# Optimization experiments

Measured on AMD Instinct MI355X. Metric: run time of the kernel, lower is better.

## Reference

```python
import jax, jax.numpy as jnp
import numpy as np


def setup_inputs() -> dict:
    key = jax.random.key(0)
    k0, k1, k2 = jax.random.split(key, 3)
    B, S, E, U = 32, 2048, 512, 512
    return {
        "seq": jax.random.normal(k0, (B, S, E), jnp.float32),
        "w1": jax.random.normal(k1, (U, E), jnp.float32) * 0.05,
        "b1": jnp.zeros((U,), jnp.float32),
        "w2": jax.random.normal(k2, (3, U), jnp.float32) * 0.05,
        "b2": jnp.zeros((3,), jnp.float32),
        "num_lists": 16,
        "list_size": 16,
    }


def reference(seq, w1, b1, w2, b2, num_lists, list_size):
    B, S, E = seq.shape
    # action decoder: Linear -> SiLU -> Linear -> Softmax over 3 actions
    h = jax.nn.silu(jnp.einsum('bse,ue->bsu', seq, w1) + b1)
    actions = jax.nn.softmax(jnp.einsum('bsu,au->bsa', h, w2) + b2, axis=-1)  # (B,S,3)

    Hn, Wn = num_lists, list_size
    T0 = jnp.zeros((B, Hn, Wn), seq.dtype).at[:, 0, -1].set(1.0)   # superposition grid
    rs0 = jnp.zeros((B, Hn), seq.dtype).at[:, 0].set(1.0)          # row sums

    # process actions in reverse token order; scan over seq dim
    acts_rev = jnp.swapaxes(actions[:, ::-1, :], 0, 1)  # (S,B,3)

    def step(carry, a):
        T, rs = carry
        a0, a1, a2 = a[:, 0:1], a[:, 1:2], a[:, 2:3]  # each (B,1)
        # weight used to place the current (reversed) token: (a0+a1)*T
        w_step = (a0 + a1)[:, :, None] * T  # (B,H,W)
        # devolve: the grouped conv2d with kernel [0, a2, a0] is a width-shift blend
        other = a2[:, :, None] * T[:, :, :-1] + a0[:, :, None] * T[:, :, 1:]  # cols 0..W-2
        sums = a1 * jnp.roll(rs, 1, axis=1).at[:, 0].set(0.0)                 # (B,H)
        last = sums + a2 * T[:, :, -1]                                        # (B,H)
        rs_new = (a0 + a2) * rs + sums
        T_new = jnp.concatenate([other, last[:, :, None]], axis=2)
        return (T_new, rs_new), w_step

    _, ws = jax.lax.scan(step, (T0, rs0), acts_rev)  # ws: (S,B,H,W), aligned with reversed seq
    # G = sum_i w_i[...,None] * token_i[:,None,None,:]
    G = jnp.einsum('sbhw,bse->bhwe', ws, seq[:, ::-1, :])
    return G
```

## Files before the change

kernel.cpp:

```cpp
#include <hip/hip_runtime.h>
#include <stdint.h>

#define S_LEN 2048
#define NB 32
#define NE 512
#define NU 512
#define NP 256

typedef __bf16 bf16;
typedef __bf16 bf16x8 __attribute__((ext_vector_type(8)));
typedef __bf16 bf16x4 __attribute__((ext_vector_type(4)));
typedef float f32x4 __attribute__((ext_vector_type(4)));
typedef float f32x8 __attribute__((ext_vector_type(8)));

__device__ __forceinline__ void gload16(const void* g, void* l) {
    __builtin_amdgcn_global_load_lds(
        (__attribute__((address_space(1))) void*)g,
        (__attribute__((address_space(3))) void*)l, 16, 0, 0);
}

__device__ __forceinline__ float dpp_shr1_z(float x) {
    return __builtin_bit_cast(float, __builtin_amdgcn_update_dpp(
        0, __builtin_bit_cast(int, x), 0x111, 0xF, 0xF, true));
}
__device__ __forceinline__ float dpp_shl1_z(float x) {
    return __builtin_bit_cast(float, __builtin_amdgcn_update_dpp(
        0, __builtin_bit_cast(int, x), 0x101, 0xF, 0xF, true));
}

__device__ __forceinline__ void stage_tile(const bf16* __restrict__ src, int SR,
                                           bf16* lds, int tid) {
#pragma unroll
    for (int rnd = 0; rnd < 2; ++rnd) {
        const int c = rnd * 256 + tid;
        const int row = c >> 2;
        const int q = (c & 3) ^ ((c >> 3) & 3);
        gload16(src + (size_t)row * SR + q * 8, lds + c * 8);
    }
}

__global__ __launch_bounds__(256) void k_wconv(
    const float* __restrict__ w1, bf16* __restrict__ wHi, bf16* __restrict__ wLo)
{
    const int i = (blockIdx.x * 256 + threadIdx.x) * 4;
    const float4 v = *(const float4*)(w1 + i);
    const float vv[4] = {v.x, v.y, v.z, v.w};
    bf16x4 oh, ol;
#pragma unroll
    for (int q = 0; q < 4; ++q) {
        const bf16 hb = (bf16)vv[q];
        oh[q] = hb;
        ol[q] = (bf16)(vv[q] - (float)hb);
    }
    *(bf16x4*)(wHi + i) = oh;
    *(bf16x4*)(wLo + i) = ol;
}

__global__ __launch_bounds__(256, 2) void k_gemm1(
    const float* __restrict__ seq,
    const bf16* __restrict__ w1H, const bf16* __restrict__ w1L,
    const float* __restrict__ b1v, const float* __restrict__ w2,
    const float* __restrict__ b2v, float* __restrict__ actions)
{
    __shared__ __align__(16) bf16 BhL[2][4096];
    __shared__ __align__(16) bf16 BlL[2][4096];
    const int tid = threadIdx.x;
    const int wid = tid >> 6;
    const int lane = tid & 63;
    const int lr = lane & 15, lg = lane >> 4;
    const int m0 = blockIdx.x << 7;

    const float* arow0 = seq + (size_t)(m0 + wid * 32 + lr) * NE + lg * 8;
    const float* arow1 = arow0 + 16 * NE;
    const int lroff = lr * 64 + (lg ^ ((lr >> 1) & 3)) * 16;

    float plog[3][2][4];
#pragma unroll
    for (int a = 0; a < 3; ++a)
#pragma unroll
        for (int i = 0; i < 2; ++i)
#pragma unroll
            for (int q = 0; q < 4; ++q) plog[a][i][q] = 0.f;

    f32x4 acc[2][8];
    stage_tile(w1H, NE, BhL[0], tid);
    stage_tile(w1L, NE, BlL[0], tid);
    f32x8 Aa0 = *(const f32x8*)(arow0);
    f32x8 Aa1 = *(const f32x8*)(arow1);
    f32x8 Ab0, Ab1;

#define G1_BODY(g, buf, Ac0, Ac1, An0, An1) do {                              \
        __syncthreads();                                                      \
        if (((g) & 15) == 0) {                                                \
            _Pragma("unroll") for (int i = 0; i < 2; ++i)                     \
            _Pragma("unroll") for (int j = 0; j < 8; ++j)                     \
                acc[i][j] = (f32x4)(0.f);                                     \
        }                                                                     \
        bf16x8 bh[8], bl[8];                                                  \
        _Pragma("unroll") for (int j = 0; j < 8; ++j) {                       \
            bh[j] = *(const bf16x8*)((const char*)BhL[buf] + j * 1024 + lroff);\
            bl[j] = *(const bf16x8*)((const char*)BlL[buf] + j * 1024 + lroff);\
        }                                                                     \
        __syncthreads();                                                      \
        if ((g) < 63) {                                                       \
            const int gn = (g) + 1;                                           \
            const int u0n = (gn >> 4) << 7;                                   \
            const int k0n = (gn & 15) << 5;                                   \
            An0 = *(const f32x8*)(arow0 + k0n);                               \
            An1 = *(const f32x8*)(arow1 + k0n);                               \
            stage_tile(w1H + (size_t)u0n * NE + k0n, NE, BhL[(buf) ^ 1], tid);\
            stage_tile(w1L + (size_t)u0n * NE + k0n, NE, BlL[(buf) ^ 1], tid);\
        }                                                                     \
        bf16x8 Ah0, Al0, Ah1, Al1;                                            \
        _Pragma("unroll") for (int q = 0; q < 8; ++q) {                       \
            const bf16 h0 = (bf16)Ac0[q];                                     \
            Ah0[q] = h0; Al0[q] = (bf16)(Ac0[q] - (float)h0);                 \
            const bf16 h1 = (bf16)Ac1[q];                                     \
            Ah1[q] = h1; Al1[q] = (bf16)(Ac1[q] - (float)h1);                 \
        }                                                                     \
        _Pragma("unroll") for (int j = 0; j < 8; ++j) {                       \
            acc[0][j] = __builtin_amdgcn_mfma_f32_16x16x32_bf16(Ah0, bh[j], acc[0][j], 0, 0, 0); \
            acc[0][j] = __builtin_amdgcn_mfma_f32_16x16x32_bf16(Ah0, bl[j], acc[0][j], 0, 0, 0); \
            acc[0][j] = __builtin_amdgcn_mfma_f32_16x16x32_bf16(Al0, bh[j], acc[0][j], 0, 0, 0); \
            acc[1][j] = __builtin_amdgcn_mfma_f32_16x16x32_bf16(Ah1, bh[j], acc[1][j], 0, 0, 0); \
            acc[1][j] = __builtin_amdgcn_mfma_f32_16x16x32_bf16(Ah1, bl[j], acc[1][j], 0, 0, 0); \
            acc[1][j] = __builtin_amdgcn_mfma_f32_16x16x32_bf16(Al1, bh[j], acc[1][j], 0, 0, 0); \
        }                                                                     \
        if (((g) & 15) == 15) {                                               \
            const int u0 = ((g) >> 4) << 7;                                   \
            _Pragma("unroll") for (int j = 0; j < 8; ++j) {                   \
                const int col = u0 + j * 16 + lr;                             \
                const float b1c = b1v[col];                                   \
                const float w20 = w2[col], w21 = w2[NU + col], w22 = w2[2 * NU + col]; \
                _Pragma("unroll") for (int i = 0; i < 2; ++i)                 \
                _Pragma("unroll") for (int q = 0; q < 4; ++q) {               \
                    const float x = acc[i][j][q] + b1c;                       \
                    const float hgate = x / (1.f + __expf(-x));               \
                    plog[0][i][q] = fmaf(hgate, w20, plog[0][i][q]);          \
                    plog[1][i][q] = fmaf(hgate, w21, plog[1][i][q]);          \
                    plog[2][i][q] = fmaf(hgate, w22, plog[2][i][q]);          \
                }                                                             \
            }                                                                 \
        }                                                                     \
    } while (0)

    for (int gg = 0; gg < 32; ++gg) {
        G1_BODY(2 * gg, 0, Aa0, Aa1, Ab0, Ab1);
        G1_BODY(2 * gg + 1, 1, Ab0, Ab1, Aa0, Aa1);
    }
#undef G1_BODY

#pragma unroll
    for (int m = 1; m < 16; m <<= 1) {
#pragma unroll
        for (int a = 0; a < 3; ++a)
#pragma unroll
            for (int i = 0; i < 2; ++i)
#pragma unroll
                for (int q = 0; q < 4; ++q)
                    plog[a][i][q] += __shfl_xor(plog[a][i][q], m);
    }
    const float bb0 = b2v[0], bb1 = b2v[1], bb2 = b2v[2];
    if (lr == 0) {
#pragma unroll
        for (int i = 0; i < 2; ++i)
#pragma unroll
            for (int q = 0; q < 4; ++q) {
                const int row = m0 + wid * 32 + i * 16 + lg * 4 + q;
                const float l0 = plog[0][i][q] + bb0;
                const float l1 = plog[1][i][q] + bb1;
                const float l2 = plog[2][i][q] + bb2;
                const float mx = fmaxf(l0, fmaxf(l1, l2));
                const float e0 = __expf(l0 - mx), e1 = __expf(l1 - mx), e2 = __expf(l2 - mx);
                const float inv = 1.f / (e0 + e1 + e2);
                *(float4*)(actions + (size_t)row * 4) = make_float4(e0 * inv, e1 * inv, e2 * inv, 0.f);
            }
    }
}

union SPMem {
    float tile[64][65];
    struct {
        float4 actbuf[3][256];
        float  sums[2][256][16];
    } s;
};

__device__ __forceinline__ void rs_chunk(const float4* __restrict__ pb,
                                         float* __restrict__ so,
                                         float& rs, int lane)
{
    for (int w = 0; w < 32; ++w) {
        const int rtop = 255 - w * 8;
        const float4 e0 = pb[rtop],     e1 = pb[rtop - 1];
        const float4 e2 = pb[rtop - 2], e3 = pb[rtop - 3];
        const float4 e4 = pb[rtop - 4], e5 = pb[rtop - 5];
        const float4 e6 = pb[rtop - 6], e7 = pb[rtop - 7];
#define RS_STEP(E, k) do {                                                    \
        const float rsp = dpp_shr1_z(rs);                                     \
        const float s = (E).y * rsp;                                          \
        if (lane < 16) so[(rtop - (k)) * 16 + lane] = s;                      \
        rs = fmaf((E).x + (E).z, rs, s);                                      \
    } while (0)
        RS_STEP(e0, 0); RS_STEP(e1, 1); RS_STEP(e2, 2); RS_STEP(e3, 3);
        RS_STEP(e4, 4); RS_STEP(e5, 5); RS_STEP(e6, 6); RS_STEP(e7, 7);
#undef RS_STEP
    }
}

__device__ __forceinline__ void t_chunk(const float4* __restrict__ lb,
                                        const float* __restrict__ sp,
                                        float& T, bf16* __restrict__ obp,
                                        int tbase0, int w15)
{
    for (int w = 0; w < 32; ++w) {
        const int rtop = 255 - w * 8;
        const int tglob = tbase0 + rtop - 7;
        const float4 av0 = lb[rtop],     av1 = lb[rtop - 1];
        const float4 av2 = lb[rtop - 2], av3 = lb[rtop - 3];
        const float4 av4 = lb[rtop - 4], av5 = lb[rtop - 5];
        const float4 av6 = lb[rtop - 6], av7 = lb[rtop - 7];
        const float su0 = sp[rtop * 16],       su1 = sp[(rtop - 1) * 16];
        const float su2 = sp[(rtop - 2) * 16], su3 = sp[(rtop - 3) * 16];
        const float su4 = sp[(rtop - 4) * 16], su5 = sp[(rtop - 5) * 16];
        const float su6 = sp[(rtop - 6) * 16], su7 = sp[(rtop - 7) * 16];
        bf16x8 fr;
#define T_STEP(Av, Su, fi) do {                                               \
        const float a0 = (Av).x, a1 = (Av).y, a2 = (Av).z;                    \
        fr[fi] = (bf16)((a0 + a1) * T);                                       \
        const float nT = dpp_shl1_z(T);                                       \
        const float contrib = w15 ? (Su) : a0 * nT;                           \
        T = fmaf(a2, T, contrib);                                             \
    } while (0)
        T_STEP(av0, su0, 7); T_STEP(av1, su1, 6);
        T_STEP(av2, su2, 5); T_STEP(av3, su3, 4);
        T_STEP(av4, su4, 3); T_STEP(av5, su5, 2);
        T_STEP(av6, su6, 1); T_STEP(av7, su7, 0);
#undef T_STEP
        *(bf16x8*)(obp + tglob) = fr;
    }
}

__global__ __launch_bounds__(320) void k_scan_prep(
    const float* __restrict__ actions, bf16* __restrict__ wsT,
    const float* __restrict__ seq, bf16* __restrict__ tHi)
{
    __shared__ SPMem sm;
    const int tid = threadIdx.x;
    if (blockIdx.x < 32) {
        const int b = blockIdx.x;
        const int wid = tid >> 6;
        const int lane = tid & 63;
        const float4* actb = (const float4*)actions + (size_t)b * S_LEN;

        float rs = (lane == 0) ? 1.f : 0.f;
        float T = (wid == 0 && lane == 15) ? 1.f : 0.f;
        const int w15 = ((lane & 15) == 15) ? 1 : 0;
        bf16* obp = wsT + ((size_t)b * NP + wid * 64 + lane) * S_LEN;

        if (wid < 4) {
            gload16(actb + 1792 + wid * 64 + lane, &sm.s.actbuf[0][wid * 64]);
            gload16(actb + 1536 + wid * 64 + lane, &sm.s.actbuf[1][wid * 64]);
            asm volatile("s_waitcnt vmcnt(0)" ::: "memory");
        }
        __syncthreads();
        if (wid == 4) rs_chunk(sm.s.actbuf[0], &sm.s.sums[0][0][0], rs, lane);
        __syncthreads();

        int bufT = 0, bufP = 1, bufL = 2;
        for (int c = 0; c < 8; ++c) {
            if (wid < 4) {
                if (c < 6)
                    gload16(actb + (1280 - c * 256) + wid * 64 + lane,
                            &sm.s.actbuf[bufL][wid * 64]);
                t_chunk(sm.s.actbuf[bufT],
                        &sm.s.sums[c & 1][0][wid * 4 + (lane >> 4)],
                        T, obp, 1792 - c * 256, w15);
                asm volatile("s_waitcnt vmcnt(0)" ::: "memory");
            } else {
                if (c < 7)
                    rs_chunk(sm.s.actbuf[bufP], &sm.s.sums[(c + 1) & 1][0][0], rs, lane);
            }
            __syncthreads();
            const int t = bufT; bufT = bufP; bufP = bufL; bufL = t;
        }
        return;
    }
    const int bid = blockIdx.x - 32;
    const int b = bid >> 8;
    const int r = bid & 255;
    const int s0 = (r & 31) << 6;
    const int e0 = (r >> 5) << 6;
    const int tx = tid & 15, ty = (tid & 255) >> 4;
    const float* src = seq + ((size_t)b * S_LEN + s0) * NE + e0;
    if (tid < 256) {
#pragma unroll
        for (int i = 0; i < 4; ++i) {
            const int row = ty + i * 16;
            const float4 v = *(const float4*)(src + (size_t)row * NE + tx * 4);
            sm.tile[row][tx * 4 + 0] = v.x; sm.tile[row][tx * 4 + 1] = v.y;
            sm.tile[row][tx * 4 + 2] = v.z; sm.tile[row][tx * 4 + 3] = v.w;
        }
    }
    __syncthreads();
    if (tid < 256) {
        const int sx = tid & 7, ey = tid >> 3;
#pragma unroll
        for (int jj = 0; jj < 2; ++jj) {
            const int er = ey + jj * 32;
            bf16x8 oh;
#pragma unroll
            for (int q = 0; q < 8; ++q) oh[q] = (bf16)sm.tile[sx * 8 + q][er];
            *(bf16x8*)(tHi + ((size_t)b * NE + e0 + er) * S_LEN + s0 + sx * 8) = oh;
        }
    }
}

__global__ __launch_bounds__(256, 2) void k_gemm2(
    const bf16* __restrict__ wsT, const bf16* __restrict__ seqtH,
    float* __restrict__ part)
{
    __shared__ __align__(16) bf16 AL[2][4096];
    __shared__ __align__(16) bf16 BL[2][4096];
    const int tid = threadIdx.x;
    const int wid = tid >> 6;
    const int lane = tid & 63;
    const int lr = lane & 15, lg = lane >> 4;
    const int bid = blockIdx.x;
    const int b = bid >> 4;
    const int sub = bid & 15;
    const int kc = sub >> 3;
    const int p0 = ((sub >> 2) & 1) << 7;
    const int e0 = (sub & 3) << 7;

    const bf16* Abase = wsT + ((size_t)b * NP + p0) * S_LEN + kc * 1024;
    const bf16* Bbase = seqtH + ((size_t)b * NE + e0) * S_LEN + kc * 1024;
    const int lroff = lr * 64 + (lg ^ ((lr >> 1) & 3)) * 16;

    f32x4 acc[2][8];
#pragma unroll
    for (int i = 0; i < 2; ++i)
#pragma unroll
        for (int j = 0; j < 8; ++j) acc[i][j] = (f32x4)(0.f);

    stage_tile(Abase, S_LEN, AL[0], tid);
    stage_tile(Bbase, S_LEN, BL[0], tid);

#define G2_BODY(kt, buf) do {                                                 \
        __syncthreads();                                                      \
        bf16x8 af[2], bfv[8];                                                 \
        _Pragma("unroll") for (int i = 0; i < 2; ++i)                         \
            af[i] = *(const bf16x8*)((const char*)AL[buf]                     \
                     + (wid * 32 + i * 16) * 64 + lroff);                     \
        _Pragma("unroll") for (int j = 0; j < 8; ++j)                         \
            bfv[j] = *(const bf16x8*)((const char*)BL[buf] + j * 1024 + lroff);\
        __syncthreads();                                                      \
        if ((kt) < 31) {                                                      \
            stage_tile(Abase + ((kt) + 1) * 32, S_LEN, AL[(buf) ^ 1], tid);   \
            stage_tile(Bbase + ((kt) + 1) * 32, S_LEN, BL[(buf) ^ 1], tid);   \
        }                                                                     \
        _Pragma("unroll") for (int j = 0; j < 8; ++j) {                       \
            acc[0][j] = __builtin_amdgcn_mfma_f32_16x16x32_bf16(af[0], bfv[j], acc[0][j], 0, 0, 0); \
            acc[1][j] = __builtin_amdgcn_mfma_f32_16x16x32_bf16(af[1], bfv[j], acc[1][j], 0, 0, 0); \
        }                                                                     \
    } while (0)

    for (int kk = 0; kk < 16; ++kk) {
        G2_BODY(2 * kk, 0);
        G2_BODY(2 * kk + 1, 1);
    }
#undef G2_BODY

    float* obp = part + (((size_t)kc * NB + b) * NP + p0 + wid * 32) * NE + e0;
#pragma unroll
    for (int i = 0; i < 2; ++i)
#pragma unroll
        for (int j = 0; j < 8; ++j)
#pragma unroll
            for (int q = 0; q < 4; ++q)
                obp[(size_t)(i * 16 + lg * 4 + q) * NE + j * 16 + lr] = acc[i][j][q];
}

__global__ __launch_bounds__(256) void k_gred(
    const float* __restrict__ part, float* __restrict__ outp)
{
    const size_t i = ((size_t)blockIdx.x * 256 + threadIdx.x) * 4;
    const float4 p0 = *(const float4*)(part + i);
    const float4 p1 = *(const float4*)(part + ((size_t)NB * NP * NE) + i);
    *(float4*)(outp + i) = make_float4(p0.x + p1.x, p0.y + p1.y,
                                       p0.z + p1.z, p0.w + p1.w);
}

extern "C" void kernel_launch(void* const* d_in, const int* in_sizes, int n_in,
                              void* d_out, int out_size, void* d_ws, size_t ws_size,
                              hipStream_t stream) {
    (void)in_sizes; (void)n_in; (void)out_size; (void)ws_size;
    const float* seq = (const float*)d_in[0];
    const float* w1  = (const float*)d_in[1];
    const float* b1  = (const float*)d_in[2];
    const float* w2  = (const float*)d_in[3];
    const float* b2  = (const float*)d_in[4];
    float* outp = (float*)d_out;

    char* ws = (char*)d_ws;
    bf16*  seqtH   = (bf16*)(ws);
    bf16*  wsT     = (bf16*)(ws + (64ull << 20));
    float* actions = (float*)(ws + (96ull << 20));
    bf16*  w1H     = (bf16*)(ws + (97ull << 20));
    bf16*  w1L     = (bf16*)(ws + (97ull << 20) + (512u << 10));
    float* part    = (float*)(ws + (98ull << 20));

    hipLaunchKernelGGL(k_wconv, dim3(256),  dim3(256), 0, stream, w1, w1H, w1L);
    hipLaunchKernelGGL(k_gemm1, dim3(512),  dim3(256), 0, stream,
                       seq, w1H, w1L, b1, w2, b2, actions);
    hipLaunchKernelGGL(k_scan_prep, dim3(32 + 8192), dim3(320), 0, stream,
                       actions, wsT, seq, seqtH);
    hipLaunchKernelGGL(k_gemm2, dim3(512),  dim3(256), 0, stream, wsT, seqtH, part);
    hipLaunchKernelGGL(k_gred,  dim3(4096), dim3(256), 0, stream, part, outp);
}
```

Before: 287.7 us.

## Move seq transpose-to-bf16 blocks from scan kernel into gemm1 launch

```diff
diff --git a/kernel.cpp b/kernel.cpp
--- a/kernel.cpp
+++ b/kernel.cpp
@@ -6,6 +6,7 @@
 #define NE 512
 #define NU 512
 #define NP 256
+#define G1_BLOCKS 512
 
 typedef __bf16 bf16;
 typedef __bf16 bf16x8 __attribute__((ext_vector_type(8)));
@@ -56,15 +57,49 @@
     *(bf16x4*)(wLo + i) = ol;
 }
 
+union G1Mem {
+    struct { bf16 BhL[2][4096]; bf16 BlL[2][4096]; } gm;
+    float tile[64][65];
+};
+
 __global__ __launch_bounds__(256, 2) void k_gemm1(
     const float* __restrict__ seq,
     const bf16* __restrict__ w1H, const bf16* __restrict__ w1L,
     const float* __restrict__ b1v, const float* __restrict__ w2,
-    const float* __restrict__ b2v, float* __restrict__ actions)
-{
-    __shared__ __align__(16) bf16 BhL[2][4096];
-    __shared__ __align__(16) bf16 BlL[2][4096];
+    const float* __restrict__ b2v, float* __restrict__ actions,
+    bf16* __restrict__ tHi)
+{
+    __shared__ __align__(16) G1Mem sm;
     const int tid = threadIdx.x;
+
+    if (blockIdx.x >= G1_BLOCKS) {
+        const int bid = blockIdx.x - G1_BLOCKS;
+        const int b = bid >> 8;
+        const int r = bid & 255;
+        const int s0 = (r & 31) << 6;
+        const int e0 = (r >> 5) << 6;
+        const int tx = tid & 15, ty = tid >> 4;
+        const float* src = seq + ((size_t)b * S_LEN + s0) * NE + e0;
+#pragma unroll
+        for (int i = 0; i < 4; ++i) {
+            const int row = ty + i * 16;
+            const float4 v = *(const float4*)(src + (size_t)row * NE + tx * 4);
+            sm.tile[row][tx * 4 + 0] = v.x; sm.tile[row][tx * 4 + 1] = v.y;
+            sm.tile[row][tx * 4 + 2] = v.z; sm.tile[row][tx * 4 + 3] = v.w;
+        }
+        __syncthreads();
+        const int sx = tid & 7, ey = tid >> 3;
+#pragma unroll
+        for (int jj = 0; jj < 2; ++jj) {
+            const int er = ey + jj * 32;
+            bf16x8 oh;
+#pragma unroll
+            for (int q = 0; q < 8; ++q) oh[q] = (bf16)sm.tile[sx * 8 + q][er];
+            *(bf16x8*)(tHi + ((size_t)b * NE + e0 + er) * S_LEN + s0 + sx * 8) = oh;
+        }
+        return;
+    }
+
     const int wid = tid >> 6;
     const int lane = tid & 63;
     const int lr = lane & 15, lg = lane >> 4;
@@ -83,8 +118,8 @@
             for (int q = 0; q < 4; ++q) plog[a][i][q] = 0.f;
 
     f32x4 acc[2][8];
-    stage_tile(w1H, NE, BhL[0], tid);
-    stage_tile(w1L, NE, BlL[0], tid);
+    stage_tile(w1H, NE, sm.gm.BhL[0], tid);
+    stage_tile(w1L, NE, sm.gm.BlL[0], tid);
     f32x8 Aa0 = *(const f32x8*)(arow0);
     f32x8 Aa1 = *(const f32x8*)(arow1);
     f32x8 Ab0, Ab1;
@@ -98,8 +133,8 @@
         }                                                                     \
         bf16x8 bh[8], bl[8];                                                  \
         _Pragma("unroll") for (int j = 0; j < 8; ++j) {                       \
-            bh[j] = *(const bf16x8*)((const char*)BhL[buf] + j * 1024 + lroff);\
-            bl[j] = *(const bf16x8*)((const char*)BlL[buf] + j * 1024 + lroff);\
+            bh[j] = *(const bf16x8*)((const char*)sm.gm.BhL[buf] + j * 1024 + lroff);\
+            bl[j] = *(const bf16x8*)((const char*)sm.gm.BlL[buf] + j * 1024 + lroff);\
         }                                                                     \
         __syncthreads();                                                      \
         if ((g) < 63) {                                                       \
@@ -108,8 +143,8 @@
             const int k0n = (gn & 15) << 5;                                   \
             An0 = *(const f32x8*)(arow0 + k0n);                               \
             An1 = *(const f32x8*)(arow1 + k0n);                               \
-            stage_tile(w1H + (size_t)u0n * NE + k0n, NE, BhL[(buf) ^ 1], tid);\
-            stage_tile(w1L + (size_t)u0n * NE + k0n, NE, BlL[(buf) ^ 1], tid);\
+            stage_tile(w1H + (size_t)u0n * NE + k0n, NE, sm.gm.BhL[(buf) ^ 1], tid);\
+            stage_tile(w1L + (size_t)u0n * NE + k0n, NE, sm.gm.BlL[(buf) ^ 1], tid);\
         }                                                                     \
         bf16x8 Ah0, Al0, Ah1, Al1;                                            \
         _Pragma("unroll") for (int q = 0; q < 8; ++q) {                       \
@@ -178,12 +213,9 @@
     }
 }
 
-union SPMem {
-    float tile[64][65];
-    struct {
-        float4 actbuf[3][256];
-        float  sums[2][256][16];
-    } s;
+struct ScanMem {
+    float4 actbuf[3][256];
+    float  sums[2][256][16];
 };
 
 __device__ __forceinline__ void rs_chunk(const float4* __restrict__ pb,
@@ -241,78 +273,46 @@
     }
 }
 
-__global__ __launch_bounds__(320) void k_scan_prep(
-    const float* __restrict__ actions, bf16* __restrict__ wsT,
-    const float* __restrict__ seq, bf16* __restrict__ tHi)
-{
-    __shared__ SPMem sm;
+__global__ __launch_bounds__(320) void k_scan(
+    const float* __restrict__ actions, bf16* __restrict__ wsT)
+{
+    __shared__ ScanMem sm;
     const int tid = threadIdx.x;
-    if (blockIdx.x < 32) {
-        const int b = blockIdx.x;
-        const int wid = tid >> 6;
-        const int lane = tid & 63;
-        const float4* actb = (const float4*)actions + (size_t)b * S_LEN;
-
-        float rs = (lane == 0) ? 1.f : 0.f;
-        float T = (wid == 0 && lane == 15) ? 1.f : 0.f;
-        const int w15 = ((lane & 15) == 15) ? 1 : 0;
-        bf16* obp = wsT + ((size_t)b * NP + wid * 64 + lane) * S_LEN;
-
+    const int b = blockIdx.x;
+    const int wid = tid >> 6;
+    const int lane = tid & 63;
+    const float4* actb = (const float4*)actions + (size_t)b * S_LEN;
+
+    float rs = (lane == 0) ? 1.f : 0.f;
+    float T = (wid == 0 && lane == 15) ? 1.f : 0.f;
+    const int w15 = ((lane & 15) == 15) ? 1 : 0;
+    bf16* obp = wsT + ((size_t)b * NP + wid * 64 + lane) * S_LEN;
+
+    if (wid < 4) {
+        gload16(actb + 1792 + wid * 64 + lane, &sm.actbuf[0][wid * 64]);
+        gload16(actb + 1536 + wid * 64 + lane, &sm.actbuf[1][wid * 64]);
+        asm volatile("s_waitcnt vmcnt(0)" ::: "memory");
+    }
+    __syncthreads();
+    if (wid == 4) rs_chunk(sm.actbuf[0], &sm.sums[0][0][0], rs, lane);
+    __syncthreads();
+
+    int bufT = 0, bufP = 1, bufL = 2;
+    for (int c = 0; c < 8; ++c) {
         if (wid < 4) {
-            gload16(actb + 1792 + wid * 64 + lane, &sm.s.actbuf[0][wid * 64]);
-            gload16(actb + 1536 + wid * 64 + lane, &sm.s.actbuf[1][wid * 64]);
+            if (c < 6)
+                gload16(actb + (1280 - c * 256) + wid * 64 + lane,
+                        &sm.actbuf[bufL][wid * 64]);
+            t_chunk(sm.actbuf[bufT],
+                    &sm.sums[c & 1][0][wid * 4 + (lane >> 4)],
+                    T, obp, 1792 - c * 256, w15);
             asm volatile("s_waitcnt vmcnt(0)" ::: "memory");
+        } else {
+            if (c < 7)
+                rs_chunk(sm.actbuf[bufP], &sm.sums[(c + 1) & 1][0][0], rs, lane);
         }
         __syncthreads();
-        if (wid == 4) rs_chunk(sm.s.actbuf[0], &sm.s.sums[0][0][0], rs, lane);
-        __syncthreads();
-
-        int bufT = 0, bufP = 1, bufL = 2;
-        for (int c = 0; c < 8; ++c) {
-            if (wid < 4) {
-                if (c < 6)
-                    gload16(actb + (1280 - c * 256) + wid * 64 + lane,
-                            &sm.s.actbuf[bufL][wid * 64]);
-                t_chunk(sm.s.actbuf[bufT],
-                        &sm.s.sums[c & 1][0][wid * 4 + (lane >> 4)],
-                        T, obp, 1792 - c * 256, w15);
-                asm volatile("s_waitcnt vmcnt(0)" ::: "memory");
-            } else {
-                if (c < 7)
-                    rs_chunk(sm.s.actbuf[bufP], &sm.s.sums[(c + 1) & 1][0][0], rs, lane);
-            }
-            __syncthreads();
-            const int t = bufT; bufT = bufP; bufP = bufL; bufL = t;
-        }
-        return;
-    }
-    const int bid = blockIdx.x - 32;
-    const int b = bid >> 8;
-    const int r = bid & 255;
-    const int s0 = (r & 31) << 6;
-    const int e0 = (r >> 5) << 6;
-    const int tx = tid & 15, ty = (tid & 255) >> 4;
-    const float* src = seq + ((size_t)b * S_LEN + s0) * NE + e0;
-    if (tid < 256) {
-#pragma unroll
-        for (int i = 0; i < 4; ++i) {
-            const int row = ty + i * 16;
-            const float4 v = *(const float4*)(src + (size_t)row * NE + tx * 4);
-            sm.tile[row][tx * 4 + 0] = v.x; sm.tile[row][tx * 4 + 1] = v.y;
-            sm.tile[row][tx * 4 + 2] = v.z; sm.tile[row][tx * 4 + 3] = v.w;
-        }
-    }
-    __syncthreads();
-    if (tid < 256) {
-        const int sx = tid & 7, ey = tid >> 3;
-#pragma unroll
-        for (int jj = 0; jj < 2; ++jj) {
-            const int er = ey + jj * 32;
-            bf16x8 oh;
-#pragma unroll
-            for (int q = 0; q < 8; ++q) oh[q] = (bf16)sm.tile[sx * 8 + q][er];
-            *(bf16x8*)(tHi + ((size_t)b * NE + e0 + er) * S_LEN + s0 + sx * 8) = oh;
-        }
+        const int t = bufT; bufT = bufP; bufP = bufL; bufL = t;
     }
 }
 
@@ -410,11 +410,10 @@
     bf16*  w1L     = (bf16*)(ws + (97ull << 20) + (512u << 10));
     float* part    = (float*)(ws + (98ull << 20));
 
-    hipLaunchKernelGGL(k_wconv, dim3(256),  dim3(256), 0, stream, w1, w1H, w1L);
-    hipLaunchKernelGGL(k_gemm1, dim3(512),  dim3(256), 0, stream,
-                       seq, w1H, w1L, b1, w2, b2, actions);
-    hipLaunchKernelGGL(k_scan_prep, dim3(32 + 8192), dim3(320), 0, stream,
-                       actions, wsT, seq, seqtH);
+    hipLaunchKernelGGL(k_wconv, dim3(256), dim3(256), 0, stream, w1, w1H, w1L);
+    hipLaunchKernelGGL(k_gemm1, dim3(G1_BLOCKS + 8192), dim3(256), 0, stream,
+                       seq, w1H, w1L, b1, w2, b2, actions, seqtH);
+    hipLaunchKernelGGL(k_scan,  dim3(32),   dim3(320), 0, stream, actions, wsT);
     hipLaunchKernelGGL(k_gemm2, dim3(512),  dim3(256), 0, stream, wsT, seqtH, part);
     hipLaunchKernelGGL(k_gred,  dim3(4096), dim3(256), 0, stream, part, outp);
 }
```

Measured after the change: 306.0 us. 1.06x slower.

## Split scan across four blocks per batch with redundant row-sum wave

Applied to the files above, without the earlier changes.

```diff
diff --git a/kernel.cpp b/kernel.cpp
--- a/kernel.cpp
+++ b/kernel.cpp
@@ -6,6 +6,7 @@
 #define NE 512
 #define NU 512
 #define NP 256
+#define SCAN_BLOCKS 128
 
 typedef __bf16 bf16;
 typedef __bf16 bf16x8 __attribute__((ext_vector_type(8)));
@@ -182,14 +183,16 @@
     float tile[64][65];
     struct {
         float4 actbuf[3][256];
-        float  sums[2][256][16];
+        float  sums[2][256][4];
     } s;
 };
 
-__device__ __forceinline__ void rs_chunk(const float4* __restrict__ pb,
-                                         float* __restrict__ so,
-                                         float& rs, int lane)
-{
+__device__ __forceinline__ void rs_chunk4(const float4* __restrict__ pb,
+                                          float* __restrict__ so,
+                                          float& rs, int lane, int hb)
+{
+    const int hl = lane - hb * 4;
+    const bool st = (lane >= hb * 4) && (lane < hb * 4 + 4);
     for (int w = 0; w < 32; ++w) {
         const int rtop = 255 - w * 8;
         const float4 e0 = pb[rtop],     e1 = pb[rtop - 1];
@@ -199,7 +202,7 @@
 #define RS_STEP(E, k) do {                                                    \
         const float rsp = dpp_shr1_z(rs);                                     \
         const float s = (E).y * rsp;                                          \
-        if (lane < 16) so[(rtop - (k)) * 16 + lane] = s;                      \
+        if (st) so[(rtop - (k)) * 4 + hl] = s;                                \
         rs = fmaf((E).x + (E).z, rs, s);                                      \
     } while (0)
         RS_STEP(e0, 0); RS_STEP(e1, 1); RS_STEP(e2, 2); RS_STEP(e3, 3);
@@ -208,10 +211,10 @@
     }
 }
 
-__device__ __forceinline__ void t_chunk(const float4* __restrict__ lb,
-                                        const float* __restrict__ sp,
-                                        float& T, bf16* __restrict__ obp,
-                                        int tbase0, int w15)
+__device__ __forceinline__ void t_chunk4(const float4* __restrict__ lb,
+                                         const float* __restrict__ sp,
+                                         float& T, bf16* __restrict__ obp,
+                                         int tbase0, int w15)
 {
     for (int w = 0; w < 32; ++w) {
         const int rtop = 255 - w * 8;
@@ -220,10 +223,10 @@
         const float4 av2 = lb[rtop - 2], av3 = lb[rtop - 3];
         const float4 av4 = lb[rtop - 4], av5 = lb[rtop - 5];
         const float4 av6 = lb[rtop - 6], av7 = lb[rtop - 7];
-        const float su0 = sp[rtop * 16],       su1 = sp[(rtop - 1) * 16];
-        const float su2 = sp[(rtop - 2) * 16], su3 = sp[(rtop - 3) * 16];
-        const float su4 = sp[(rtop - 4) * 16], su5 = sp[(rtop - 5) * 16];
-        const float su6 = sp[(rtop - 6) * 16], su7 = sp[(rtop - 7) * 16];
+        const float su0 = sp[rtop * 4],       su1 = sp[(rtop - 1) * 4];
+        const float su2 = sp[(rtop - 2) * 4], su3 = sp[(rtop - 3) * 4];
+        const float su4 = sp[(rtop - 4) * 4], su5 = sp[(rtop - 5) * 4];
+        const float su6 = sp[(rtop - 6) * 4], su7 = sp[(rtop - 7) * 4];
         bf16x8 fr;
 #define T_STEP(Av, Su, fi) do {                                               \
         const float a0 = (Av).x, a1 = (Av).y, a2 = (Av).z;                    \
@@ -241,78 +244,69 @@
     }
 }
 
-__global__ __launch_bounds__(320) void k_scan_prep(
+__global__ __launch_bounds__(256) void k_scan_prep(
     const float* __restrict__ actions, bf16* __restrict__ wsT,
     const float* __restrict__ seq, bf16* __restrict__ tHi)
 {
     __shared__ SPMem sm;
     const int tid = threadIdx.x;
-    if (blockIdx.x < 32) {
-        const int b = blockIdx.x;
+    if (blockIdx.x < SCAN_BLOCKS) {
+        const int b = blockIdx.x >> 2;
+        const int hb = blockIdx.x & 3;
         const int wid = tid >> 6;
         const int lane = tid & 63;
         const float4* actb = (const float4*)actions + (size_t)b * S_LEN;
 
         float rs = (lane == 0) ? 1.f : 0.f;
-        float T = (wid == 0 && lane == 15) ? 1.f : 0.f;
+        float T = (hb == 0 && wid == 0 && lane == 15) ? 1.f : 0.f;
         const int w15 = ((lane & 15) == 15) ? 1 : 0;
-        bf16* obp = wsT + ((size_t)b * NP + wid * 64 + lane) * S_LEN;
-
-        if (wid < 4) {
-            gload16(actb + 1792 + wid * 64 + lane, &sm.s.actbuf[0][wid * 64]);
-            gload16(actb + 1536 + wid * 64 + lane, &sm.s.actbuf[1][wid * 64]);
-            asm volatile("s_waitcnt vmcnt(0)" ::: "memory");
-        }
+        bf16* obp = wsT + ((size_t)b * NP + hb * 64 + lane) * S_LEN;
+
+        gload16(actb + 1792 + tid, &sm.s.actbuf[0][tid]);
+        gload16(actb + 1536 + tid, &sm.s.actbuf[1][tid]);
+        asm volatile("s_waitcnt vmcnt(0)" ::: "memory");
         __syncthreads();
-        if (wid == 4) rs_chunk(sm.s.actbuf[0], &sm.s.sums[0][0][0], rs, lane);
+        if (wid == 1) rs_chunk4(sm.s.actbuf[0], &sm.s.sums[0][0][0], rs, lane, hb);
         __syncthreads();
 
         int bufT = 0, bufP = 1, bufL = 2;
         for (int c = 0; c < 8; ++c) {
-            if (wid < 4) {
-                if (c < 6)
-                    gload16(actb + (1280 - c * 256) + wid * 64 + lane,
-                            &sm.s.actbuf[bufL][wid * 64]);
-                t_chunk(sm.s.actbuf[bufT],
-                        &sm.s.sums[c & 1][0][wid * 4 + (lane >> 4)],
-                        T, obp, 1792 - c * 256, w15);
-                asm volatile("s_waitcnt vmcnt(0)" ::: "memory");
-            } else {
-                if (c < 7)
-                    rs_chunk(sm.s.actbuf[bufP], &sm.s.sums[(c + 1) & 1][0][0], rs, lane);
-            }
+            if (c < 6)
+                gload16(actb + (1280 - c * 256) + tid, &sm.s.actbuf[bufL][tid]);
+            if (wid == 0)
+                t_chunk4(sm.s.actbuf[bufT], &sm.s.sums[c & 1][0][lane >> 4],
+                         T, obp, 1792 - c * 256, w15);
+            else if (wid == 1 && c < 7)
+                rs_chunk4(sm.s.actbuf[bufP], &sm.s.sums[(c + 1) & 1][0][0], rs, lane, hb);
+            asm volatile("s_waitcnt vmcnt(0)" ::: "memory");
             __syncthreads();
             const int t = bufT; bufT = bufP; bufP = bufL; bufL = t;
         }
         return;
     }
-    const int bid = blockIdx.x - 32;
+    const int bid = blockIdx.x - SCAN_BLOCKS;
     const int b = bid >> 8;
     const int r = bid & 255;
     const int s0 = (r & 31) << 6;
     const int e0 = (r >> 5) << 6;
-    const int tx = tid & 15, ty = (tid & 255) >> 4;
+    const int tx = tid & 15, ty = tid >> 4;
     const float* src = seq + ((size_t)b * S_LEN + s0) * NE + e0;
-    if (tid < 256) {
-#pragma unroll
-        for (int i = 0; i < 4; ++i) {
-            const int row = ty + i * 16;
-            const float4 v = *(const float4*)(src + (size_t)row * NE + tx * 4);
-            sm.tile[row][tx * 4 + 0] = v.x; sm.tile[row][tx * 4 + 1] = v.y;
-            sm.tile[row][tx * 4 + 2] = v.z; sm.tile[row][tx * 4 + 3] = v.w;
-        }
+#pragma unroll
+    for (int i = 0; i < 4; ++i) {
+        const int row = ty + i * 16;
+        const float4 v = *(const float4*)(src + (size_t)row * NE + tx * 4);
+        sm.tile[row][tx * 4 + 0] = v.x; sm.tile[row][tx * 4 + 1] = v.y;
+        sm.tile[row][tx * 4 + 2] = v.z; sm.tile[row][tx * 4 + 3] = v.w;
     }
     __syncthreads();
-    if (tid < 256) {
-        const int sx = tid & 7, ey = tid >> 3;
-#pragma unroll
-        for (int jj = 0; jj < 2; ++jj) {
-            const int er = ey + jj * 32;
-            bf16x8 oh;
-#pragma unroll
-            for (int q = 0; q < 8; ++q) oh[q] = (bf16)sm.tile[sx * 8 + q][er];
-            *(bf16x8*)(tHi + ((size_t)b * NE + e0 + er) * S_LEN + s0 + sx * 8) = oh;
-        }
+    const int sx = tid & 7, ey = tid >> 3;
+#pragma unroll
+    for (int jj = 0; jj < 2; ++jj) {
+        const int er = ey + jj * 32;
+        bf16x8 oh;
+#pragma unroll
+        for (int q = 0; q < 8; ++q) oh[q] = (bf16)sm.tile[sx * 8 + q][er];
+        *(bf16x8*)(tHi + ((size_t)b * NE + e0 + er) * S_LEN + s0 + sx * 8) = oh;
     }
 }
 
@@ -410,10 +404,10 @@
     bf16*  w1L     = (bf16*)(ws + (97ull << 20) + (512u << 10));
     float* part    = (float*)(ws + (98ull << 20));
 
-    hipLaunchKernelGGL(k_wconv, dim3(256),  dim3(256), 0, stream, w1, w1H, w1L);
-    hipLaunchKernelGGL(k_gemm1, dim3(512),  dim3(256), 0, stream,
+    hipLaunchKernelGGL(k_wconv, dim3(256), dim3(256), 0, stream, w1, w1H, w1L);
+    hipLaunchKernelGGL(k_gemm1, dim3(512), dim3(256), 0, stream,
                        seq, w1H, w1L, b1, w2, b2, actions);
-    hipLaunchKernelGGL(k_scan_prep, dim3(32 + 8192), dim3(320), 0, stream,
+    hipLaunchKernelGGL(k_scan_prep, dim3(SCAN_BLOCKS + 8192), dim3(256), 0, stream,
                        actions, wsT, seq, seqtH);
     hipLaunchKernelGGL(k_gemm2, dim3(512),  dim3(256), 0, stream, wsT, seqtH, part);
     hipLaunchKernelGGL(k_gred,  dim3(4096), dim3(256), 0, stream, part, outp);
```

After: 284.8 us. No clear change (-1.0%).
